# Kernel tuning notes

Measured on AMD Instinct MI355X. Metric: run time of the kernel, lower is better.

## Reference

```python
import jax, jax.numpy as jnp
import numpy as np

NUM_TAGS = 20000
H_DIM = 256
EPS = 1e-5


def _layernorm(x, g, b):
    mu = x.mean(-1, keepdims=True)
    var = ((x - mu) ** 2).mean(-1, keepdims=True)
    return (x - mu) * jax.lax.rsqrt(var + EPS) * g + b


def setup_inputs() -> dict:
    key = jax.random.key(0)
    ks = jax.random.split(key, 16)
    B, F, T = 64, 128, 16
    h4 = H_DIM * 4
    s = 0.02
    return {
        "tags": jax.random.randint(ks[0], (B, F, T), 0, NUM_TAGS),
        "feature_counts": jax.random.uniform(ks[1], (B,), jnp.float32) * 100.0,
        # tag_norm LayerNorm(num_tags)
        "ln_g": jnp.ones((NUM_TAGS,), jnp.float32),
        "ln_b": jnp.zeros((NUM_TAGS,), jnp.float32),
        # encoder: Linear(num_tags+1 -> 4h), GELU, LayerNorm(4h), MLP(4h->4h->h)
        "w1": jax.random.normal(ks[2], (NUM_TAGS + 1, h4), jnp.float32) * s,
        "b1": jnp.zeros((h4,), jnp.float32),
        "ln2_g": jnp.ones((h4,), jnp.float32),
        "ln2_b": jnp.zeros((h4,), jnp.float32),
        "we1": jax.random.normal(ks[3], (h4, h4), jnp.float32) * s,
        "be1": jnp.zeros((h4,), jnp.float32),
        "we2": jax.random.normal(ks[4], (h4, H_DIM), jnp.float32) * s,
        "be2": jnp.zeros((H_DIM,), jnp.float32),
        # decoder: MLP(h -> 4h -> num_tags+1)
        "wd1": jax.random.normal(ks[5], (H_DIM, h4), jnp.float32) * s,
        "bd1": jnp.zeros((h4,), jnp.float32),
        "wd2": jax.random.normal(ks[6], (h4, NUM_TAGS + 1), jnp.float32) * s,
        "bd2": jnp.zeros((NUM_TAGS + 1,), jnp.float32),
    }


def reference(tags, feature_counts, ln_g, ln_b, w1, b1, ln2_g, ln2_b,
              we1, be1, we2, be2, wd1, bd1, wd2, bd2):
    B, F, T = tags.shape
    # multi_hot.scatter_(2, tags, 1).clamp_(0,1): duplicates within a row collapse to 1
    bi = jnp.arange(B)[:, None, None]
    fi = jnp.arange(F)[None, :, None]
    multi_hot = jnp.zeros((B, F, NUM_TAGS), jnp.float32).at[bi, fi, tags].set(1.0)
    tile_tag_count = multi_hot.sum(axis=1)  # [B, num_tags]

    yn = _layernorm(tile_tag_count, ln_g, ln_b)
    y = jnp.concatenate([feature_counts[:, None] / 100.0, yn], axis=1)  # [B, num_tags+1]

    # encoder
    h = jax.nn.gelu(y @ w1 + b1, approximate=False)
    h = _layernorm(h, ln2_g, ln2_b)
    h = jax.nn.gelu(h @ we1 + be1, approximate=False)
    enc = h @ we2 + be2  # [B, h_dim]

    # decoder
    d = jax.nn.gelu(enc @ wd1 + bd1, approximate=False)
    dec = d @ wd2 + bd2  # [B, num_tags+1]
    return (y, enc, dec)
```

## Files before the change

kernel.cpp:

```cpp
#include <hip/hip_runtime.h>
#include <math.h>

#define NUM_TAGS 20000
#define BATCH 64
#define H4 1024
#define HD 256
#define NT1 20001

__device__ __forceinline__ float gelu_exact(float x) {
    return 0.5f * x * (1.0f + erff(x * 0.7071067811865476f));
}

struct F4 { float x, y, z, w; };

typedef const __attribute__((address_space(1))) void* gp_t;
typedef __attribute__((address_space(3))) void* lp_t;
__device__ __forceinline__ void async_ld4(const float* g, float* lds_base) {
    __builtin_amdgcn_global_load_lds((gp_t)g, (lp_t)lds_base, 4, 0, 0);
}
__device__ __forceinline__ void async_ld16(const float* g, float* lds_base) {
    __builtin_amdgcn_global_load_lds((gp_t)g, (lp_t)lds_base, 16, 0, 0);
}

__global__ __launch_bounds__(1024) void k_ln1_fused(const int* __restrict__ tags,
                                                    const float* __restrict__ fc,
                                                    const float* __restrict__ lng,
                                                    const float* __restrict__ lnb,
                                                    float* __restrict__ y) {
    __shared__ int hist[NUM_TAGS];
    __shared__ float ls[16], ls2[16], smu, srs;
    const int b = blockIdx.x, tid = threadIdx.x;

    for (int t = tid; t < NUM_TAGS; t += 1024) hist[t] = 0;
    __syncthreads();

    if (tid < 128) {
        const int* tp = tags + ((size_t)(b * 128 + tid) << 4);
        int t[16];
#pragma unroll
        for (int i = 0; i < 16; ++i) t[i] = tp[i];
#pragma unroll
        for (int i = 0; i < 16; ++i) {
            bool dup = false;
            for (int j = 0; j < i; ++j) dup = dup || (t[j] == t[i]);
            if (!dup) atomicAdd(&hist[t[i]], 1);
        }
    }
    __syncthreads();

    float s = 0.f, s2 = 0.f;
    for (int t = tid; t < NUM_TAGS; t += 1024) {
        float v = (float)hist[t];
        s += v; s2 += v * v;
    }
#pragma unroll
    for (int off = 32; off > 0; off >>= 1) {
        s  += __shfl_down(s, off);
        s2 += __shfl_down(s2, off);
    }
    int wave = tid >> 6;
    if ((tid & 63) == 0) { ls[wave] = s; ls2[wave] = s2; }
    __syncthreads();
    if (tid == 0) {
        float S = 0.f, S2 = 0.f;
#pragma unroll
        for (int i = 0; i < 16; ++i) { S += ls[i]; S2 += ls2[i]; }
        float mu = S / (float)NUM_TAGS;
        float var = S2 / (float)NUM_TAGS - mu * mu;
        smu = mu;
        srs = rsqrtf(var + 1e-5f);
    }
    __syncthreads();
    float mu = smu, rs = srs;

    float* yrow = y + (size_t)b * NT1;
    if (tid == 0) yrow[0] = fc[b] * 0.01f;
    for (int t = tid; t < NUM_TAGS; t += 1024) {
        float v = (float)hist[t];
        yrow[1 + t] = (v - mu) * rs * lng[t] + lnb[t];
    }
}

template <int PATH>
__global__ __launch_bounds__(256, 2) void k_gemm(const float* __restrict__ A, int lda,
                                                 const float* __restrict__ W, int ldw,
                                                 float* __restrict__ P,
                                                 int N, int kpb) {
    __shared__ __align__(16) float As[4][512];
    __shared__ __align__(16) float Ws[4][2048];
    const int tid = threadIdx.x;
    const int lane = tid & 63, wid = tid >> 6;
    const int tn = tid & 31, tb = tid >> 5;
    const int n0 = blockIdx.x * 256;
    const int kstart = blockIdx.y * kpb;
    const int nchunk = kpb >> 3;

    float acc[8][8];
#pragma unroll
    for (int i = 0; i < 8; ++i)
#pragma unroll
        for (int j = 0; j < 8; ++j) acc[i][j] = 0.f;

    auto issue = [&](int b, int c) {
        int k0 = kstart + c * 8;
#pragma unroll
        for (int j = 0; j < 2; ++j) {
            int d0 = j * 256 + wid * 64;
            int d = d0 + lane;
            async_ld4(A + (size_t)(d >> 3) * lda + k0 + (d & 7), &As[b][d0]);
        }
        if (PATH == 0) {
#pragma unroll
            for (int j = 0; j < 2; ++j) {
                int g0 = j * 256 + wid * 64;
                int g = g0 + lane;
                int kk = g >> 6, c4 = g & 63;
                async_ld16(W + (size_t)(k0 + kk) * ldw + n0 + c4 * 4, &Ws[b][g0 * 4]);
            }
        } else {
#pragma unroll
            for (int j = 0; j < 8; ++j) {
                int d0 = j * 256 + wid * 64;
                int d = d0 + lane;
                int kk = d >> 8, cc = d & 255;
                async_ld4(W + (size_t)(k0 + kk) * ldw + min(n0 + cc, N - 1), &Ws[b][d0]);
            }
        }
    };

    issue(0, 0);
    if (nchunk > 1) issue(1, 1);

    for (int c = 0; c < nchunk; ++c) {
        if (c + 2 < nchunk) issue((c + 2) & 3, c + 2);
        int ahead = nchunk - 1 - c;
        if (PATH == 0) {
            if (ahead >= 2)      asm volatile("s_waitcnt vmcnt(8)"  ::: "memory");
            else if (ahead == 1) asm volatile("s_waitcnt vmcnt(4)"  ::: "memory");
            else                 asm volatile("s_waitcnt vmcnt(0)"  ::: "memory");
        } else {
            if (ahead >= 2)      asm volatile("s_waitcnt vmcnt(20)" ::: "memory");
            else if (ahead == 1) asm volatile("s_waitcnt vmcnt(10)" ::: "memory");
            else                 asm volatile("s_waitcnt vmcnt(0)"  ::: "memory");
        }
        __builtin_amdgcn_s_barrier();
        asm volatile("" ::: "memory");

        const float* Ab = As[c & 3];
        const float* Wb = Ws[c & 3];
        __builtin_amdgcn_s_setprio(1);
#pragma unroll
        for (int k4 = 0; k4 < 2; ++k4) {
            float4 a4[8];
#pragma unroll
            for (int i = 0; i < 8; ++i)
                a4[i] = *(const float4*)&Ab[(tb * 8 + i) * 8 + k4 * 4];
#pragma unroll
            for (int kl = 0; kl < 4; ++kl) {
                const float4 w0 = *(const float4*)&Wb[(k4 * 4 + kl) * 256 + tn * 4];
                const float4 w1 = *(const float4*)&Wb[(k4 * 4 + kl) * 256 + 128 + tn * 4];
                const float wv[8] = {w0.x, w0.y, w0.z, w0.w, w1.x, w1.y, w1.z, w1.w};
#pragma unroll
                for (int i = 0; i < 8; ++i) {
                    float av = (kl == 0) ? a4[i].x : (kl == 1) ? a4[i].y
                             : (kl == 2) ? a4[i].z : a4[i].w;
#pragma unroll
                    for (int jj = 0; jj < 8; ++jj)
                        acc[i][jj] = fmaf(av, wv[jj], acc[i][jj]);
                }
            }
        }
        __builtin_amdgcn_s_setprio(0);
        asm volatile("" ::: "memory");
    }

    float* Pp = P + ((size_t)blockIdx.x * gridDim.y + blockIdx.y) * 16384;
#pragma unroll
    for (int i = 0; i < 8; ++i) {
        int row = tb * 8 + i;
        float4 v0 = {acc[i][0], acc[i][1], acc[i][2], acc[i][3]};
        float4 v1 = {acc[i][4], acc[i][5], acc[i][6], acc[i][7]};
        *(float4*)&Pp[row * 256 + tn * 4]       = v0;
        *(float4*)&Pp[row * 256 + 128 + tn * 4] = v1;
    }
}

template <bool GELU>
__global__ __launch_bounds__(256) void k_reduce(const float* __restrict__ P, int KS,
                                                const float* __restrict__ bias,
                                                const float* __restrict__ r1row,
                                                const float* __restrict__ fc,
                                                float* __restrict__ out, int ldo, int N) {
    int b = blockIdx.y;
    int n = blockIdx.x * 256 + threadIdx.x;
    if (n >= N) return;
    int nb = n >> 8, col = n & 255;
    const float* p = P + (size_t)nb * KS * 16384 + b * 256 + col;
    float s0 = 0.f, s1 = 0.f, s2 = 0.f, s3 = 0.f;
    int k = 0;
    for (; k + 3 < KS; k += 4) {
        s0 += p[(size_t)(k + 0) * 16384];
        s1 += p[(size_t)(k + 1) * 16384];
        s2 += p[(size_t)(k + 2) * 16384];
        s3 += p[(size_t)(k + 3) * 16384];
    }
    for (; k < KS; ++k) s0 += p[(size_t)k * 16384];
    float s = (s0 + s1) + (s2 + s3) + bias[n];
    if (r1row) s += fc[b] * 0.01f * r1row[n];
    if (GELU) s = gelu_exact(s);
    out[(size_t)b * ldo + n] = s;
}

__global__ __launch_bounds__(256) void k_reduce_v4(const float* __restrict__ P, int KS,
                                                   const float* __restrict__ bias,
                                                   float* __restrict__ out, int ldo, int N) {
    int b = blockIdx.y;
    int n = (blockIdx.x * 256 + threadIdx.x) * 4;
    if (n >= N) return;
    int nb = n >> 8, col = n & 255;
    const float* p = P + (size_t)nb * KS * 16384 + b * 256 + col;
    if (n + 3 < N) {
        float sx = 0.f, sy = 0.f, sz = 0.f, sw = 0.f;
        for (int k = 0; k < KS; ++k) {
            float4 v = *(const float4*)&p[(size_t)k * 16384];
            sx += v.x; sy += v.y; sz += v.z; sw += v.w;
        }
        F4 bi = *(const F4*)&bias[n];
        F4 r = {sx + bi.x, sy + bi.y, sz + bi.z, sw + bi.w};
        *(F4*)&out[(size_t)b * ldo + n] = r;
    } else {
        for (int j = 0; n + j < N; ++j) {
            float s = 0.f;
            for (int k = 0; k < KS; ++k) s += p[(size_t)k * 16384 + j];
            out[(size_t)b * ldo + n + j] = s + bias[n + j];
        }
    }
}

__global__ __launch_bounds__(256) void k_ln2(const float* __restrict__ g1,
                                             const float* __restrict__ lng,
                                             const float* __restrict__ lnb,
                                             float* __restrict__ h2) {
    int b = blockIdx.x, tid = threadIdx.x;
    float v[4];
    float s = 0.f, s2 = 0.f;
#pragma unroll
    for (int j = 0; j < 4; ++j) {
        int nidx = tid + 256 * j;
        float x = g1[b * H4 + nidx];
        v[j] = x;
        s += x; s2 += x * x;
    }
#pragma unroll
    for (int off = 32; off > 0; off >>= 1) {
        s  += __shfl_down(s, off);
        s2 += __shfl_down(s2, off);
    }
    __shared__ float ls[4], ls2[4], smu, srs;
    int wave = tid >> 6;
    if ((tid & 63) == 0) { ls[wave] = s; ls2[wave] = s2; }
    __syncthreads();
    if (tid == 0) {
        float S  = ls[0] + ls[1] + ls[2] + ls[3];
        float S2 = ls2[0] + ls2[1] + ls2[2] + ls2[3];
        float mu = S / (float)H4;
        float var = S2 / (float)H4 - mu * mu;
        smu = mu;
        srs = rsqrtf(var + 1e-5f);
    }
    __syncthreads();
    float mu = smu, rs = srs;
#pragma unroll
    for (int j = 0; j < 4; ++j) {
        int nidx = tid + 256 * j;
        h2[b * H4 + nidx] = (v[j] - mu) * rs * lng[nidx] + lnb[nidx];
    }
}

extern "C" void kernel_launch(void* const* d_in, const int* in_sizes, int n_in,
                              void* d_out, int out_size, void* d_ws, size_t ws_size,
                              hipStream_t stream) {
    (void)in_sizes; (void)n_in; (void)out_size;
    const int*   tags  = (const int*)d_in[0];
    const float* fc    = (const float*)d_in[1];
    const float* ln_g  = (const float*)d_in[2];
    const float* ln_b  = (const float*)d_in[3];
    const float* w1    = (const float*)d_in[4];
    const float* b1    = (const float*)d_in[5];
    const float* ln2_g = (const float*)d_in[6];
    const float* ln2_b = (const float*)d_in[7];
    const float* we1   = (const float*)d_in[8];
    const float* be1   = (const float*)d_in[9];
    const float* we2   = (const float*)d_in[10];
    const float* be2   = (const float*)d_in[11];
    const float* wd1   = (const float*)d_in[12];
    const float* bd1   = (const float*)d_in[13];
    const float* wd2   = (const float*)d_in[14];
    const float* bd2   = (const float*)d_in[15];

    float* out = (float*)d_out;
    float* y   = out;
    float* enc = out + (size_t)BATCH * NT1;
    float* dec = enc + BATCH * HD;

    char* ws = (char*)d_ws;
    size_t off = 0;
    float* g1     = (float*)(ws + off); off += (size_t)BATCH * H4 * 4;
    float* h2     = (float*)(ws + off); off += (size_t)BATCH * H4 * 4;
    float* g2     = (float*)(ws + off); off += (size_t)BATCH * H4 * 4;
    float* dd     = (float*)(ws + off); off += (size_t)BATCH * H4 * 4;
    float* arena  = (float*)(ws + off);
    size_t avail  = (ws_size > off) ? (ws_size - off) : 0;

    const size_t MB = 1024 * 1024;
    int KS5;
    if (avail >= 45 * MB)      { KS5 = 8; }
    else if (avail >= 33 * MB) { KS5 = 4; }
    else if (avail >= 17 * MB) { KS5 = 4; }
    else                       { KS5 = 2; }
    int kpb5 = H4 / KS5;

    k_ln1_fused<<<64, 1024, 0, stream>>>(tags, fc, ln_g, ln_b, y);

    k_gemm<0><<<dim3(4, 125), 256, 0, stream>>>(y + 1, NT1, w1 + H4, H4, arena, H4, 160);
    k_reduce<true><<<dim3(4, 64), 256, 0, stream>>>(arena, 125, b1, w1, fc, g1, H4, H4);
    k_ln2<<<64, 256, 0, stream>>>(g1, ln2_g, ln2_b, h2);

    k_gemm<0><<<dim3(4, 32), 256, 0, stream>>>(h2, H4, we1, H4, arena, H4, 32);
    k_reduce<true><<<dim3(4, 64), 256, 0, stream>>>(arena, 32, be1, nullptr, nullptr, g2, H4, H4);

    k_gemm<0><<<dim3(1, 32), 256, 0, stream>>>(g2, H4, we2, HD, arena, HD, 32);
    k_reduce<false><<<dim3(1, 64), 256, 0, stream>>>(arena, 32, be2, nullptr, nullptr, enc, HD, HD);

    k_gemm<0><<<dim3(4, 16), 256, 0, stream>>>(enc, HD, wd1, H4, arena, H4, 16);
    k_reduce<true><<<dim3(4, 64), 256, 0, stream>>>(arena, 16, bd1, nullptr, nullptr, dd, H4, H4);

    k_gemm<1><<<dim3(79, KS5), 256, 0, stream>>>(dd, H4, wd2, NT1, arena, NT1, kpb5);
    k_reduce_v4<<<dim3(20, 64), 256, 0, stream>>>(arena, KS5, bd2, dec, NT1, NT1);
}
```

Baseline: 320.1 us.

## Halve GEMM N-tile to 128 columns and fuse first reduce with LayerNorm

```diff
diff --git a/kernel.cpp b/kernel.cpp
--- a/kernel.cpp
+++ b/kernel.cpp
@@ -87,17 +87,17 @@
                                                  float* __restrict__ P,
                                                  int N, int kpb) {
     __shared__ __align__(16) float As[4][512];
-    __shared__ __align__(16) float Ws[4][2048];
+    __shared__ __align__(16) float Ws[4][1024];
     const int tid = threadIdx.x;
     const int lane = tid & 63, wid = tid >> 6;
-    const int tn = tid & 31, tb = tid >> 5;
-    const int n0 = blockIdx.x * 256;
+    const int tn = tid & 15, tb = tid >> 4;
+    const int n0 = blockIdx.x * 128;
     const int kstart = blockIdx.y * kpb;
     const int nchunk = kpb >> 3;
 
-    float acc[8][8];
-#pragma unroll
-    for (int i = 0; i < 8; ++i)
+    float acc[4][8];
+#pragma unroll
+    for (int i = 0; i < 4; ++i)
 #pragma unroll
         for (int j = 0; j < 8; ++j) acc[i][j] = 0.f;
 
@@ -107,23 +107,19 @@
         for (int j = 0; j < 2; ++j) {
             int d0 = j * 256 + wid * 64;
             int d = d0 + lane;
-            async_ld4(A + (size_t)(d >> 3) * lda + k0 + (d & 7), &As[b][d0]);
+            int k4 = d >> 8, row = (d & 255) >> 2, klo = d & 3;
+            async_ld4(A + (size_t)row * lda + k0 + k4 * 4 + klo, &As[b][d0]);
         }
         if (PATH == 0) {
-#pragma unroll
-            for (int j = 0; j < 2; ++j) {
-                int g0 = j * 256 + wid * 64;
-                int g = g0 + lane;
-                int kk = g >> 6, c4 = g & 63;
-                async_ld16(W + (size_t)(k0 + kk) * ldw + n0 + c4 * 4, &Ws[b][g0 * 4]);
-            }
+            int kk = tid >> 5, c4 = tid & 31;
+            async_ld16(W + (size_t)(k0 + kk) * ldw + n0 + c4 * 4, &Ws[b][wid * 256]);
         } else {
 #pragma unroll
-            for (int j = 0; j < 8; ++j) {
-                int d0 = j * 256 + wid * 64;
-                int d = d0 + lane;
-                int kk = d >> 8, cc = d & 255;
-                async_ld4(W + (size_t)(k0 + kk) * ldw + min(n0 + cc, N - 1), &Ws[b][d0]);
+            for (int j = 0; j < 4; ++j) {
+                int d = j * 256 + tid;
+                int kk = d >> 7, cc = d & 127;
+                async_ld4(W + (size_t)(k0 + kk) * ldw + min(n0 + cc, N - 1),
+                          &Ws[b][j * 256 + wid * 64]);
             }
         }
     };
@@ -135,12 +131,12 @@
         if (c + 2 < nchunk) issue((c + 2) & 3, c + 2);
         int ahead = nchunk - 1 - c;
         if (PATH == 0) {
-            if (ahead >= 2)      asm volatile("s_waitcnt vmcnt(8)"  ::: "memory");
-            else if (ahead == 1) asm volatile("s_waitcnt vmcnt(4)"  ::: "memory");
+            if (ahead >= 2)      asm volatile("s_waitcnt vmcnt(6)"  ::: "memory");
+            else if (ahead == 1) asm volatile("s_waitcnt vmcnt(3)"  ::: "memory");
             else                 asm volatile("s_waitcnt vmcnt(0)"  ::: "memory");
         } else {
-            if (ahead >= 2)      asm volatile("s_waitcnt vmcnt(20)" ::: "memory");
-            else if (ahead == 1) asm volatile("s_waitcnt vmcnt(10)" ::: "memory");
+            if (ahead >= 2)      asm volatile("s_waitcnt vmcnt(12)" ::: "memory");
+            else if (ahead == 1) asm volatile("s_waitcnt vmcnt(6)"  ::: "memory");
             else                 asm volatile("s_waitcnt vmcnt(0)"  ::: "memory");
         }
         __builtin_amdgcn_s_barrier();
@@ -151,22 +147,26 @@
         __builtin_amdgcn_s_setprio(1);
 #pragma unroll
         for (int k4 = 0; k4 < 2; ++k4) {
-            float4 a4[8];
-#pragma unroll
-            for (int i = 0; i < 8; ++i)
-                a4[i] = *(const float4*)&Ab[(tb * 8 + i) * 8 + k4 * 4];
+            float4 a4[4];
+#pragma unroll
+            for (int i = 0; i < 4; ++i)
+                a4[i] = *(const float4*)&Ab[k4 * 256 + (tb * 4 + i) * 4];
 #pragma unroll
             for (int kl = 0; kl < 4; ++kl) {
-                const float4 w0 = *(const float4*)&Wb[(k4 * 4 + kl) * 256 + tn * 4];
-                const float4 w1 = *(const float4*)&Wb[(k4 * 4 + kl) * 256 + 128 + tn * 4];
-                const float wv[8] = {w0.x, w0.y, w0.z, w0.w, w1.x, w1.y, w1.z, w1.w};
-#pragma unroll
-                for (int i = 0; i < 8; ++i) {
+                const float4 w0 = *(const float4*)&Wb[(k4 * 4 + kl) * 128 + tn * 4];
+                const float4 w1 = *(const float4*)&Wb[(k4 * 4 + kl) * 128 + 64 + tn * 4];
+#pragma unroll
+                for (int i = 0; i < 4; ++i) {
                     float av = (kl == 0) ? a4[i].x : (kl == 1) ? a4[i].y
                              : (kl == 2) ? a4[i].z : a4[i].w;
-#pragma unroll
-                    for (int jj = 0; jj < 8; ++jj)
-                        acc[i][jj] = fmaf(av, wv[jj], acc[i][jj]);
+                    acc[i][0] = fmaf(av, w0.x, acc[i][0]);
+                    acc[i][1] = fmaf(av, w0.y, acc[i][1]);
+                    acc[i][2] = fmaf(av, w0.z, acc[i][2]);
+                    acc[i][3] = fmaf(av, w0.w, acc[i][3]);
+                    acc[i][4] = fmaf(av, w1.x, acc[i][4]);
+                    acc[i][5] = fmaf(av, w1.y, acc[i][5]);
+                    acc[i][6] = fmaf(av, w1.z, acc[i][6]);
+                    acc[i][7] = fmaf(av, w1.w, acc[i][7]);
                 }
             }
         }
@@ -174,41 +174,83 @@
         asm volatile("" ::: "memory");
     }
 
-    float* Pp = P + ((size_t)blockIdx.x * gridDim.y + blockIdx.y) * 16384;
-#pragma unroll
-    for (int i = 0; i < 8; ++i) {
-        int row = tb * 8 + i;
+    float* Pp = P + ((size_t)blockIdx.x * gridDim.y + blockIdx.y) * 8192;
+#pragma unroll
+    for (int i = 0; i < 4; ++i) {
+        int row = tb * 4 + i;
         float4 v0 = {acc[i][0], acc[i][1], acc[i][2], acc[i][3]};
         float4 v1 = {acc[i][4], acc[i][5], acc[i][6], acc[i][7]};
-        *(float4*)&Pp[row * 256 + tn * 4]       = v0;
-        *(float4*)&Pp[row * 256 + 128 + tn * 4] = v1;
+        *(float4*)&Pp[row * 128 + tn * 4]      = v0;
+        *(float4*)&Pp[row * 128 + 64 + tn * 4] = v1;
     }
 }
 
 template <bool GELU>
 __global__ __launch_bounds__(256) void k_reduce(const float* __restrict__ P, int KS,
                                                 const float* __restrict__ bias,
-                                                const float* __restrict__ r1row,
-                                                const float* __restrict__ fc,
                                                 float* __restrict__ out, int ldo, int N) {
     int b = blockIdx.y;
     int n = blockIdx.x * 256 + threadIdx.x;
     if (n >= N) return;
-    int nb = n >> 8, col = n & 255;
-    const float* p = P + (size_t)nb * KS * 16384 + b * 256 + col;
+    int nb = n >> 7, col = n & 127;
+    const float* p = P + (size_t)nb * KS * 8192 + b * 128 + col;
     float s0 = 0.f, s1 = 0.f, s2 = 0.f, s3 = 0.f;
     int k = 0;
     for (; k + 3 < KS; k += 4) {
-        s0 += p[(size_t)(k + 0) * 16384];
-        s1 += p[(size_t)(k + 1) * 16384];
-        s2 += p[(size_t)(k + 2) * 16384];
-        s3 += p[(size_t)(k + 3) * 16384];
-    }
-    for (; k < KS; ++k) s0 += p[(size_t)k * 16384];
+        s0 += p[(size_t)(k + 0) * 8192];
+        s1 += p[(size_t)(k + 1) * 8192];
+        s2 += p[(size_t)(k + 2) * 8192];
+        s3 += p[(size_t)(k + 3) * 8192];
+    }
+    for (; k < KS; ++k) s0 += p[(size_t)k * 8192];
     float s = (s0 + s1) + (s2 + s3) + bias[n];
-    if (r1row) s += fc[b] * 0.01f * r1row[n];
     if (GELU) s = gelu_exact(s);
     out[(size_t)b * ldo + n] = s;
+}
+
+__global__ __launch_bounds__(1024) void k_red_ln2(const float* __restrict__ P, int KS,
+                                                  const float* __restrict__ bias,
+                                                  const float* __restrict__ r1row,
+                                                  const float* __restrict__ fc,
+                                                  const float* __restrict__ lng,
+                                                  const float* __restrict__ lnb,
+                                                  float* __restrict__ h2) {
+    const int b = blockIdx.x, n = threadIdx.x;
+    int nb = n >> 7, col = n & 127;
+    const float* p = P + (size_t)nb * KS * 8192 + b * 128 + col;
+    float s0 = 0.f, s1 = 0.f, s2v = 0.f, s3 = 0.f;
+    int k = 0;
+    for (; k + 3 < KS; k += 4) {
+        s0  += p[(size_t)(k + 0) * 8192];
+        s1  += p[(size_t)(k + 1) * 8192];
+        s2v += p[(size_t)(k + 2) * 8192];
+        s3  += p[(size_t)(k + 3) * 8192];
+    }
+    for (; k < KS; ++k) s0 += p[(size_t)k * 8192];
+    float v = (s0 + s1) + (s2v + s3) + bias[n] + fc[b] * 0.01f * r1row[n];
+    v = gelu_exact(v);
+
+    float s = v, s2 = v * v;
+#pragma unroll
+    for (int off = 32; off > 0; off >>= 1) {
+        s  += __shfl_down(s, off);
+        s2 += __shfl_down(s2, off);
+    }
+    __shared__ float ls[16], ls2[16], smu, srs;
+    int wave = n >> 6;
+    if ((n & 63) == 0) { ls[wave] = s; ls2[wave] = s2; }
+    __syncthreads();
+    if (n == 0) {
+        float S = 0.f, S2 = 0.f;
+#pragma unroll
+        for (int i = 0; i < 16; ++i) { S += ls[i]; S2 += ls2[i]; }
+        float mu = S / (float)H4;
+        float var = S2 / (float)H4 - mu * mu;
+        smu = mu;
+        srs = rsqrtf(var + 1e-5f);
+    }
+    __syncthreads();
+    h2[(size_t)b * H4 + n] = (v - smu) * srs * lng[n] + lnb[n];
 }
 
 __global__ __launch_bounds__(256) void k_reduce_v4(const float* __restrict__ P, int KS,
@@ -217,12 +259,12 @@
     int b = blockIdx.y;
     int n = (blockIdx.x * 256 + threadIdx.x) * 4;
     if (n >= N) return;
-    int nb = n >> 8, col = n & 255;
-    const float* p = P + (size_t)nb * KS * 16384 + b * 256 + col;
+    int nb = n >> 7, col = n & 127;
+    const float* p = P + (size_t)nb * KS * 8192 + b * 128 + col;
     if (n + 3 < N) {
         float sx = 0.f, sy = 0.f, sz = 0.f, sw = 0.f;
         for (int k = 0; k < KS; ++k) {
-            float4 v = *(const float4*)&p[(size_t)k * 16384];
+            float4 v = *(const float4*)&p[(size_t)k * 8192];
             sx += v.x; sy += v.y; sz += v.z; sw += v.w;
         }
         F4 bi = *(const F4*)&bias[n];
@@ -231,49 +273,9 @@
     } else {
         for (int j = 0; n + j < N; ++j) {
             float s = 0.f;
-            for (int k = 0; k < KS; ++k) s += p[(size_t)k * 16384 + j];
+            for (int k = 0; k < KS; ++k) s += p[(size_t)k * 8192 + j];
             out[(size_t)b * ldo + n + j] = s + bias[n + j];
         }
-    }
-}
-
-__global__ __launch_bounds__(256) void k_ln2(const float* __restrict__ g1,
-                                             const float* __restrict__ lng,
-                                             const float* __restrict__ lnb,
-                                             float* __restrict__ h2) {
-    int b = blockIdx.x, tid = threadIdx.x;
-    float v[4];
-    float s = 0.f, s2 = 0.f;
-#pragma unroll
-    for (int j = 0; j < 4; ++j) {
-        int nidx = tid + 256 * j;
-        float x = g1[b * H4 + nidx];
-        v[j] = x;
-        s += x; s2 += x * x;
-    }
-#pragma unroll
-    for (int off = 32; off > 0; off >>= 1) {
-        s  += __shfl_down(s, off);
-        s2 += __shfl_down(s2, off);
-    }
-    __shared__ float ls[4], ls2[4], smu, srs;
-    int wave = tid >> 6;
-    if ((tid & 63) == 0) { ls[wave] = s; ls2[wave] = s2; }
-    __syncthreads();
-    if (tid == 0) {
-        float S  = ls[0] + ls[1] + ls[2] + ls[3];
-        float S2 = ls2[0] + ls2[1] + ls2[2] + ls2[3];
-        float mu = S / (float)H4;
-        float var = S2 / (float)H4 - mu * mu;
-        smu = mu;
-        srs = rsqrtf(var + 1e-5f);
-    }
-    __syncthreads();
-    float mu = smu, rs = srs;
-#pragma unroll
-    for (int j = 0; j < 4; ++j) {
-        int nidx = tid + 256 * j;
-        h2[b * H4 + nidx] = (v[j] - mu) * rs * lng[nidx] + lnb[nidx];
     }
 }
 
@@ -305,7 +307,6 @@
 
     char* ws = (char*)d_ws;
     size_t off = 0;
-    float* g1     = (float*)(ws + off); off += (size_t)BATCH * H4 * 4;
     float* h2     = (float*)(ws + off); off += (size_t)BATCH * H4 * 4;
     float* g2     = (float*)(ws + off); off += (size_t)BATCH * H4 * 4;
     float* dd     = (float*)(ws + off); off += (size_t)BATCH * H4 * 4;
@@ -316,25 +317,23 @@
     int KS5;
     if (avail >= 45 * MB)      { KS5 = 8; }
     else if (avail >= 33 * MB) { KS5 = 4; }
-    else if (avail >= 17 * MB) { KS5 = 4; }
     else                       { KS5 = 2; }
     int kpb5 = H4 / KS5;
 
     k_ln1_fused<<<64, 1024, 0, stream>>>(tags, fc, ln_g, ln_b, y);
 
-    k_gemm<0><<<dim3(4, 125), 256, 0, stream>>>(y + 1, NT1, w1 + H4, H4, arena, H4, 160);
-    k_reduce<true><<<dim3(4, 64), 256, 0, stream>>>(arena, 125, b1, w1, fc, g1, H4, H4);
-    k_ln2<<<64, 256, 0, stream>>>(g1, ln2_g, ln2_b, h2);
-
-    k_gemm<0><<<dim3(4, 32), 256, 0, stream>>>(h2, H4, we1, H4, arena, H4, 32);
-    k_reduce<true><<<dim3(4, 64), 256, 0, stream>>>(arena, 32, be1, nullptr, nullptr, g2, H4, H4);
-
-    k_gemm<0><<<dim3(1, 32), 256, 0, stream>>>(g2, H4, we2, HD, arena, HD, 32);
-    k_reduce<false><<<dim3(1, 64), 256, 0, stream>>>(arena, 32, be2, nullptr, nullptr, enc, HD, HD);
-
-    k_gemm<0><<<dim3(4, 16), 256, 0, stream>>>(enc, HD, wd1, H4, arena, H4, 16);
-    k_reduce<true><<<dim3(4, 64), 256, 0, stream>>>(arena, 16, bd1, nullptr, nullptr, dd, H4, H4);
-
-    k_gemm<1><<<dim3(79, KS5), 256, 0, stream>>>(dd, H4, wd2, NT1, arena, NT1, kpb5);
+    k_gemm<0><<<dim3(8, 125), 256, 0, stream>>>(y + 1, NT1, w1 + H4, H4, arena, H4, 160);
+    k_red_ln2<<<64, 1024, 0, stream>>>(arena, 125, b1, w1, fc, ln2_g, ln2_b, h2);
+
+    k_gemm<0><<<dim3(8, 32), 256, 0, stream>>>(h2, H4, we1, H4, arena, H4, 32);
+    k_reduce<true><<<dim3(4, 64), 256, 0, stream>>>(arena, 32, be1, g2, H4, H4);
+
+    k_gemm<0><<<dim3(2, 64), 256, 0, stream>>>(g2, H4, we2, HD, arena, HD, 16);
+    k_reduce<false><<<dim3(1, 64), 256, 0, stream>>>(arena, 64, be2, enc, HD, HD);
+
+    k_gemm<0><<<dim3(8, 16), 256, 0, stream>>>(enc, HD, wd1, H4, arena, H4, 16);
+    k_reduce<true><<<dim3(4, 64), 256, 0, stream>>>(arena, 16, bd1, dd, H4, H4);
+
+    k_gemm<1><<<dim3(157, KS5), 256, 0, stream>>>(dd, H4, wd2, NT1, arena, NT1, kpb5);
     k_reduce_v4<<<dim3(20, 64), 256, 0, stream>>>(arena, KS5, bd2, dec, NT1, NT1);
 }
```

After: 314.9 us. About the same (-1.6%).
